# Optimization experiments

Measured on AMD Instinct MI355X. Metric: run time of the kernel, lower is better.

The kernel has to match this reference:

```python
import jax, jax.numpy as jnp
import numpy as np

N_APP = 100000
N_ATTR = 50000
E = 500000
D_IN = 128
D_H = 128
D_OUT = 2


def _sage(h_src, h_dst, src, dst, ew, W_self, W_neigh, b, n_dst):
    # DGL SAGEConv('mean') with edge_weight: m_e = ew_e * h_src[src_e];
    # h_neigh_v = sum_e->v m_e / in_degree(v); out = h_dst@W_self + h_neigh@W_neigh + b
    # (feat_drop=0.2 is identity in eval mode)
    m = h_src[src] * ew[:, None]                                   # [E, d]
    s = jax.ops.segment_sum(m, dst, num_segments=n_dst)            # [n_dst, d]
    deg = jax.ops.segment_sum(jnp.ones_like(ew), dst, num_segments=n_dst)
    h_neigh = s / jnp.maximum(deg, 1.0)[:, None]
    return h_dst @ W_self + h_neigh @ W_neigh + b


def _forward(x_app, x_attr, ew0, ew1, ew2,
             Wself1, Wneigh1, b1, Wself2, Wneigh2, b2, Wc, bc,
             src0, dst0, src1, dst1, src2, dst2):
    # ---- layer 1 (HeteroGraphConv, aggregate='sum' over relations per dst ntype) ----
    h_attr = _sage(x_app, x_attr, src0, dst0, ew0, Wself1[0], Wneigh1[0], b1[0], N_ATTR)
    h_app = (_sage(x_attr, x_app, src1, dst1, ew1, Wself1[1], Wneigh1[1], b1[1], N_APP)
             + _sage(x_app, x_app, src2, dst2, ew2, Wself1[2], Wneigh1[2], b1[2], N_APP))
    h_attr = jax.nn.relu(h_attr)
    h_app = jax.nn.relu(h_app)
    # ---- layer 2 ----
    h_attr2 = _sage(h_app, h_attr, src0, dst0, ew0, Wself2[0], Wneigh2[0], b2[0], N_ATTR)
    h_app2 = (_sage(h_attr, h_app, src1, dst1, ew1, Wself2[1], Wneigh2[1], b2[1], N_APP)
              + _sage(h_app, h_app, src2, dst2, ew2, Wself2[2], Wneigh2[2], b2[2], N_APP))
    del h_attr2  # second layer output on 'attribute' is unused by classify
    # ---- classify on 'application' ----
    return h_app2 @ Wc + bc


def setup_inputs() -> dict:
    key = jax.random.key(0)
    ks = jax.random.split(key, 20)
    sc = 1.0 / np.sqrt(D_H)
    return {
        "x_app": jax.random.normal(ks[0], (N_APP, D_IN), jnp.float32),
        "x_attr": jax.random.normal(ks[1], (N_ATTR, D_IN), jnp.float32),
        "ew0": jax.random.uniform(ks[2], (E,), jnp.float32),
        "ew1": jax.random.uniform(ks[3], (E,), jnp.float32),
        "ew2": jax.random.uniform(ks[4], (E,), jnp.float32),
        "Wself1": jax.random.normal(ks[5], (3, D_IN, D_H), jnp.float32) * sc,
        "Wneigh1": jax.random.normal(ks[6], (3, D_IN, D_H), jnp.float32) * sc,
        "b1": jax.random.normal(ks[7], (3, D_H), jnp.float32) * 0.01,
        "Wself2": jax.random.normal(ks[8], (3, D_H, D_H), jnp.float32) * sc,
        "Wneigh2": jax.random.normal(ks[9], (3, D_H, D_H), jnp.float32) * sc,
        "b2": jax.random.normal(ks[10], (3, D_H), jnp.float32) * 0.01,
        "Wc": jax.random.normal(ks[11], (D_H, D_OUT), jnp.float32) * sc,
        "bc": jax.random.normal(ks[12], (D_OUT,), jnp.float32) * 0.01,
        "src0": jax.random.randint(ks[13], (E,), 0, N_APP, jnp.int32),
        "dst0": jax.random.randint(ks[14], (E,), 0, N_ATTR, jnp.int32),
        "src1": jax.random.randint(ks[15], (E,), 0, N_ATTR, jnp.int32),
        "dst1": jax.random.randint(ks[16], (E,), 0, N_APP, jnp.int32),
        "src2": jax.random.randint(ks[17], (E,), 0, N_APP, jnp.int32),
        "dst2": jax.random.randint(ks[18], (E,), 0, N_APP, jnp.int32),
    }


def reference(x_app, x_attr, ew0, ew1, ew2,
              Wself1, Wneigh1, b1, Wself2, Wneigh2, b2, Wc, bc,
              src0, dst0, src1, dst1, src2, dst2):
    return _forward(x_app, x_attr, ew0, ew1, ew2,
                    Wself1, Wneigh1, b1, Wself2, Wneigh2, b2, Wc, bc,
                    src0, dst0, src1, dst1, src2, dst2)
```

## Files before the change

kernel.cpp:

```cpp
#include <hip/hip_runtime.h>

#define NAPP  100000
#define NATTR 50000
#define NE    500000
#define D     128
#define NTOT  (NATTR + 2 * NAPP)
#define SCHUNK 1024
#define SNB   ((NTOT + SCHUNK - 1) / SCHUNK)
#define EG4   ((NE / 4 + 255) / 256)
#define GB_APP  ((NAPP + 63) / 64)
#define GB_ATTR ((NATTR + 63) / 64)
#define ECAP  1024

typedef __attribute__((ext_vector_type(8))) short bfrag;
typedef __attribute__((ext_vector_type(4))) float f32x4;

__device__ __forceinline__ short bf16_rn(float x) {
    union { float f; unsigned u; } a; a.f = x;
    unsigned r = (a.u + 0x7fffu + ((a.u >> 16) & 1u)) >> 16;
    return (short)r;
}
__device__ __forceinline__ float bf16_to_f(short s) {
    union { float f; unsigned u; } a;
    a.u = ((unsigned)(unsigned short)s) << 16;
    return a.f;
}

__device__ __forceinline__ void split2(float x, float y, unsigned& hw, unsigned& lw) {
    union { float f; unsigned u; } ax, ay;
    ax.f = x; ay.f = y;
    unsigned hx = (ax.u + 0x7fffu + ((ax.u >> 16) & 1u)) >> 16;
    unsigned hy = (ay.u + 0x7fffu + ((ay.u >> 16) & 1u)) >> 16;
    union { unsigned u; float f; } fx, fy;
    fx.u = hx << 16; fy.u = hy << 16;
    union { float f; unsigned u; } rx, ry;
    rx.f = x - fx.f; ry.f = y - fy.f;
    unsigned lx = (rx.u + 0x7fffu + ((rx.u >> 16) & 1u)) >> 16;
    unsigned ly = (ry.u + 0x7fffu + ((ry.u >> 16) & 1u)) >> 16;
    hw = (hy << 16) | (hx & 0xffffu);
    lw = (ly << 16) | (lx & 0xffffu);
}

__global__ __launch_bounds__(256) void hist3_kernel(
        const int* __restrict__ d0, const int* __restrict__ d1, const int* __restrict__ d2,
        int* __restrict__ h0, int* __restrict__ h1, int* __restrict__ h2,
        int* __restrict__ r0, int* __restrict__ r1, int* __restrict__ r2) {
    int b = blockIdx.x;
    int rel = b / EG4;
    int i4 = (b - rel * EG4) * 256 + threadIdx.x;
    if (i4 * 4 >= NE) return;
    const int* dst = (rel == 0) ? d0 : (rel == 1) ? d1 : d2;
    int* h = (rel == 0) ? h0 : (rel == 1) ? h1 : h2;
    int* rk = (rel == 0) ? r0 : (rel == 1) ? r1 : r2;
    int4 d = *((const int4*)dst + i4);
    int4 r;
    r.x = atomicAdd(&h[d.x], 1);
    r.y = atomicAdd(&h[d.y], 1);
    r.z = atomicAdd(&h[d.z], 1);
    r.w = atomicAdd(&h[d.w], 1);
    *((int4*)rk + i4) = r;
}

__global__ __launch_bounds__(256) void scan_partial_kernel(const int* __restrict__ cur,
                                                           int* __restrict__ bsum) {
    int b = blockIdx.x, t = threadIdx.x;
    int4 v = *((const int4*)(cur + b * SCHUNK) + t);
    int s = v.x + v.y + v.z + v.w;
    __shared__ int sd[256];
    sd[t] = s;
    __syncthreads();
    for (int off = 128; off > 0; off >>= 1) {
        if (t < off) sd[t] += sd[t + off];
        __syncthreads();
    }
    if (t == 0) bsum[b] = sd[0];
}

__global__ __launch_bounds__(256) void scan_offsets_kernel(const int* __restrict__ bsum,
        int* __restrict__ boff, int* __restrict__ rp0, int* __restrict__ rp1,
        int* __restrict__ rp2) {
    int t = threadIdx.x;
    int v = (t < SNB) ? bsum[t] : 0;
    __shared__ int sd[256];
    sd[t] = v;
    __syncthreads();
    for (int off = 1; off < 256; off <<= 1) {
        int u = (t >= off) ? sd[t - off] : 0;
        __syncthreads();
        sd[t] += u;
        __syncthreads();
    }
    boff[t] = sd[t] - v;
    if (t == 0) { rp0[NATTR] = NE; rp1[NAPP] = NE; rp2[NAPP] = NE; }
}

__global__ __launch_bounds__(256) void scan_final_kernel(const int* __restrict__ cur,
        const int* __restrict__ boff, int* __restrict__ rp0, int* __restrict__ rp1,
        int* __restrict__ rp2) {
    int b = blockIdx.x, t = threadIdx.x;
    int base = b * SCHUNK + t * 4;
    int4 v = *(const int4*)(cur + base);
    int s = v.x + v.y + v.z + v.w;
    __shared__ int sd[256];
    sd[t] = s;
    __syncthreads();
    for (int off = 1; off < 256; off <<= 1) {
        int u = (t >= off) ? sd[t - off] : 0;
        __syncthreads();
        sd[t] += u;
        __syncthreads();
    }
    int pre = boff[b] + sd[t] - s;
    int ex[4];
    ex[0] = pre;
    ex[1] = ex[0] + v.x;
    ex[2] = ex[1] + v.y;
    ex[3] = ex[2] + v.z;
    #pragma unroll
    for (int i = 0; i < 4; i++) {
        int idx = base + i;
        if (idx < NTOT) {
            int* rp; int loc; int rbase;
            if (idx < NATTR)             { rp = rp0; loc = idx;                 rbase = 0; }
            else if (idx < NATTR + NAPP) { rp = rp1; loc = idx - NATTR;        rbase = NE; }
            else                         { rp = rp2; loc = idx - NATTR - NAPP; rbase = 2 * NE; }
            rp[loc] = ex[i] - rbase;
        }
    }
}

__global__ __launch_bounds__(256) void scatter3_kernel(
        const int* __restrict__ s0, const int* __restrict__ d0, const float* __restrict__ e0,
        const int* __restrict__ r0, const int* __restrict__ rp0, int2* __restrict__ cw0,
        const int* __restrict__ s1, const int* __restrict__ d1, const float* __restrict__ e1,
        const int* __restrict__ r1, const int* __restrict__ rp1, int2* __restrict__ cw1,
        const int* __restrict__ s2, const int* __restrict__ d2, const float* __restrict__ e2,
        const int* __restrict__ r2, const int* __restrict__ rp2, int2* __restrict__ cw2) {
    int b = blockIdx.x;
    int rel = b / EG4;
    int i4 = (b - rel * EG4) * 256 + threadIdx.x;
    if (i4 * 4 >= NE) return;
    const int* src; const int* dst; const float* ew; const int* rk; const int* rp; int2* cw;
    if (rel == 0)      { src = s0; dst = d0; ew = e0; rk = r0; rp = rp0; cw = cw0; }
    else if (rel == 1) { src = s1; dst = d1; ew = e1; rk = r1; rp = rp1; cw = cw1; }
    else               { src = s2; dst = d2; ew = e2; rk = r2; rp = rp2; cw = cw2; }
    int4 s = *((const int4*)src + i4);
    int4 d = *((const int4*)dst + i4);
    float4 e = *((const float4*)ew + i4);
    int4 r = *((const int4*)rk + i4);
    cw[rp[d.x] + r.x] = make_int2(s.x, __float_as_int(e.x));
    cw[rp[d.y] + r.y] = make_int2(s.y, __float_as_int(e.y));
    cw[rp[d.z] + r.z] = make_int2(s.z, __float_as_int(e.z));
    cw[rp[d.w] + r.w] = make_int2(s.w, __float_as_int(e.w));
}

__global__ __launch_bounds__(256) void pack_kernel(
        const float* __restrict__ Wself1, const float* __restrict__ Wneigh1,
        const float* __restrict__ Wself2, const float* __restrict__ Wneigh2,
        const float* __restrict__ b1, const float* __restrict__ b2,
        const float* __restrict__ Wc, const float* __restrict__ bc,
        short* __restrict__ PBh, short* __restrict__ PBl,
        float* __restrict__ b1s, float* __restrict__ b2s,
        float* __restrict__ Cs, float* __restrict__ C1, float* __restrict__ C2,
        float* __restrict__ bconst) {
    int m = blockIdx.x;
    if (m == 8) {
        int tid = threadIdx.x;
        int k = tid >> 1, j = tid & 1;
        const float* Wn1 = Wneigh2 + D * D;
        const float* Wn2 = Wneigh2 + 2 * D * D;
        const float* Ws1 = Wself2 + D * D;
        const float* Ws2 = Wself2 + 2 * D * D;
        float ss = 0.f, s1 = 0.f, s2 = 0.f;
        for (int tt = 0; tt < D; tt++) {
            float wc = Wc[tt * 2 + j];
            ss += (Ws1[k * D + tt] + Ws2[k * D + tt]) * wc;
            s1 += Wn1[k * D + tt] * wc;
            s2 += Wn2[k * D + tt] * wc;
        }
        Cs[tid] = ss; C1[tid] = s1; C2[tid] = s2;
        if (tid < 2) {
            float s = bc[tid];
            for (int tt = 0; tt < D; tt++)
                s += (b2[D + tt] + b2[2 * D + tt]) * Wc[tt * 2 + tid];
            bconst[tid] = s;
        }
        return;
    }
    const float* srcA; const float* srcB = nullptr;
    switch (m) {
        case 0: srcA = Wself1; break;
        case 1: srcA = Wneigh1; break;
        case 2: srcA = Wself1 + D * D; srcB = Wself1 + 2 * D * D; break;
        case 3: srcA = Wneigh1 + D * D; break;
        case 4: srcA = Wneigh1 + 2 * D * D; break;
        case 5: srcA = Wself2 + D * D; srcB = Wself2 + 2 * D * D; break;
        case 6: srcA = Wneigh2 + D * D; break;
        default: srcA = Wneigh2 + 2 * D * D; break;
    }
    short* oh = PBh + (size_t)m * D * D;
    short* ol = PBl + (size_t)m * D * D;
    for (int i = threadIdx.x; i < D * D; i += 256) {
        int k = i >> 7, n = i & 127;
        float v = srcA[i];
        if (srcB) v += srcB[i];
        short hi = bf16_rn(v);
        short lo = bf16_rn(v - bf16_to_f(hi));
        int kc = k >> 5, q = (k >> 3) & 3, j = k & 7, nt = n >> 4, c = n & 15;
        int pos = (((kc * 8 + nt) * 64) + q * 16 + c) * 8 + j;
        oh[pos] = hi;
        ol[pos] = lo;
    }
    if (m == 0 && threadIdx.x < D) {
        int t = threadIdx.x;
        b1s[t] = b1[D + t] + b1[2 * D + t];
        b2s[t] = b2[D + t] + b2[2 * D + t];
    }
}

#define ASTR 128
template<int NG>
__device__ __forceinline__ void fused_body(
        const float* __restrict__ in0, const short* __restrict__ B0h, const short* __restrict__ B0l,
        const float* __restrict__ x1, const int* __restrict__ rp1, const int2* __restrict__ cw1,
        const short* __restrict__ B1h, const short* __restrict__ B1l,
        const float* __restrict__ x2, const int* __restrict__ rp2, const int2* __restrict__ cw2,
        const short* __restrict__ B2h, const short* __restrict__ B2l,
        const float* __restrict__ bias,
        const float* __restrict__ Ccol0, const float* __restrict__ Ccol1,
        float* __restrict__ zo0, float* __restrict__ zo1,
        int nrows, int row0, float* At, int2* eds) {
    const int t = threadIdx.x;
    const int w = t >> 6, lane = t & 63;
    const int q = lane >> 4, c = lane & 15;
    const int myrow = row0 + w * 16 + c;
    const int arow = min(myrow, nrows - 1);

    f32x4 acc[8];
    #pragma unroll
    for (int nt = 0; nt < 8; nt++) acc[nt] = (f32x4){0.f, 0.f, 0.f, 0.f};

    {
        const float* __restrict__ arp = in0 + (size_t)arow * D;
        const bfrag* __restrict__ Bh = (const bfrag*)B0h;
        const bfrag* __restrict__ Bl = (const bfrag*)B0l;
        #pragma unroll
        for (int kc = 0; kc < 4; kc++) {
            float4 a0 = *(const float4*)(arp + kc * 32 + q * 8);
            float4 a1 = *(const float4*)(arp + kc * 32 + q * 8 + 4);
            union { unsigned u[4]; bfrag v; } ahu, alu;
            split2(a0.x, a0.y, ahu.u[0], alu.u[0]);
            split2(a0.z, a0.w, ahu.u[1], alu.u[1]);
            split2(a1.x, a1.y, ahu.u[2], alu.u[2]);
            split2(a1.z, a1.w, ahu.u[3], alu.u[3]);
            bfrag ah = ahu.v, al = alu.v;
            const bfrag* bh = Bh + kc * 512 + lane;
            const bfrag* bl = Bl + kc * 512 + lane;
            #pragma unroll
            for (int nt = 0; nt < 8; nt++) {
                bfrag vh = bh[nt * 64];
                bfrag vl = bl[nt * 64];
                acc[nt] = __builtin_amdgcn_mfma_f32_16x16x32_bf16(ah, vh, acc[nt], 0, 0, 0);
                acc[nt] = __builtin_amdgcn_mfma_f32_16x16x32_bf16(ah, vl, acc[nt], 0, 0, 0);
                acc[nt] = __builtin_amdgcn_mfma_f32_16x16x32_bf16(al, vh, acc[nt], 0, 0, 0);
            }
        }
    }

    const int grp = t >> 5, l32 = t & 31;
    #pragma unroll
    for (int g = 0; g < NG; g++) {
        const float* __restrict__ xs = (g == 0) ? x1 : x2;
        const int* __restrict__ rp   = (g == 0) ? rp1 : rp2;
        const int2* __restrict__ cw  = (g == 0) ? cw1 : cw2;
        const short* __restrict__ Bhp = (g == 0) ? B1h : B2h;
        const short* __restrict__ Blp = (g == 0) ? B1l : B2l;

        if (g > 0) __syncthreads();
        const int eb0 = rp[row0];
        const int eb1 = rp[min(row0 + 64, nrows)];
        const int ecnt = eb1 - eb0;
        const bool staged = (ecnt < ECAP);
        if (staged) {
            for (int i = t; i < ecnt; i += 256) eds[i] = cw[eb0 + i];
            if (t == 0) eds[ecnt] = make_int2(0, 0);
        }
        __syncthreads();

        {
            const int r0g = row0 + grp * 8;
            int bnd[9];
            #pragma unroll
            for (int i = 0; i < 9; i++) bnd[i] = rp[min(r0g + i, nrows)];
            #pragma unroll
            for (int p = 0; p < 4; p++) {
                const int A0 = bnd[2 * p],     A1 = bnd[2 * p + 1];
                const int B0 = bnd[2 * p + 1], B1 = bnd[2 * p + 2];
                float4 aA = make_float4(0.f, 0.f, 0.f, 0.f);
                float4 aB = make_float4(0.f, 0.f, 0.f, 0.f);
                const int lastA = min(max(A1 - 1, A0), NE - 1);
                const int lastB = min(max(B1 - 1, B0), NE - 1);
                int jA = A0, jB = B0;
                while (jA < A1 || jB < B1) {
                    int2 ed[8];
                    if (staged) {
                        #pragma unroll
                        for (int u = 0; u < 4; u++)
                            ed[u] = eds[min(min(jA + u, lastA) - eb0, ecnt)];
                        #pragma unroll
                        for (int u = 0; u < 4; u++)
                            ed[4 + u] = eds[min(min(jB + u, lastB) - eb0, ecnt)];
                    } else {
                        #pragma unroll
                        for (int u = 0; u < 4; u++) ed[u] = cw[min(jA + u, lastA)];
                        #pragma unroll
                        for (int u = 0; u < 4; u++) ed[4 + u] = cw[min(jB + u, lastB)];
                    }
                    float wt[8];
                    #pragma unroll
                    for (int u = 0; u < 4; u++)
                        wt[u] = (jA + u < A1) ? __int_as_float(ed[u].y) : 0.f;
                    #pragma unroll
                    for (int u = 0; u < 4; u++)
                        wt[4 + u] = (jB + u < B1) ? __int_as_float(ed[4 + u].y) : 0.f;
                    float4 v[8];
                    #pragma unroll
                    for (int u = 0; u < 8; u++)
                        v[u] = *(const float4*)(xs + (size_t)ed[u].x * D + l32 * 4);
                    aA.x += wt[0] * v[0].x + wt[1] * v[1].x + wt[2] * v[2].x + wt[3] * v[3].x;
                    aA.y += wt[0] * v[0].y + wt[1] * v[1].y + wt[2] * v[2].y + wt[3] * v[3].y;
                    aA.z += wt[0] * v[0].z + wt[1] * v[1].z + wt[2] * v[2].z + wt[3] * v[3].z;
                    aA.w += wt[0] * v[0].w + wt[1] * v[1].w + wt[2] * v[2].w + wt[3] * v[3].w;
                    aB.x += wt[4] * v[4].x + wt[5] * v[5].x + wt[6] * v[6].x + wt[7] * v[7].x;
                    aB.y += wt[4] * v[4].y + wt[5] * v[5].y + wt[6] * v[6].y + wt[7] * v[7].y;
                    aB.z += wt[4] * v[4].z + wt[5] * v[5].z + wt[6] * v[6].z + wt[7] * v[7].z;
                    aB.w += wt[4] * v[4].w + wt[5] * v[5].w + wt[6] * v[6].w + wt[7] * v[7].w;
                    jA += 4; jB += 4;
                }
                const float invA = 1.0f / (float)max(A1 - A0, 1);
                const float invB = 1.0f / (float)max(B1 - B0, 1);
                aA.x *= invA; aA.y *= invA; aA.z *= invA; aA.w *= invA;
                aB.x *= invB; aB.y *= invB; aB.z *= invB; aB.w *= invB;
                const int lrA = grp * 8 + 2 * p;
                const int lrB = lrA + 1;
                *(float4*)&At[lrA * ASTR + ((l32 ^ ((lrA & 3) << 1)) << 2)] = aA;
                *(float4*)&At[lrB * ASTR + ((l32 ^ ((lrB & 3) << 1)) << 2)] = aB;
            }
        }
        __syncthreads();

        const bfrag* __restrict__ Bh = (const bfrag*)Bhp;
        const bfrag* __restrict__ Bl = (const bfrag*)Blp;
        const int rloc = w * 16 + c;
        const int sw = (rloc & 3) << 1;
        const float* __restrict__ arow_lds = &At[rloc * ASTR];
        #pragma unroll
        for (int kc = 0; kc < 4; kc++) {
            const int g0 = kc * 8 + q * 2;
            float4 a0 = *(const float4*)(arow_lds + ((g0 ^ sw) << 2));
            float4 a1 = *(const float4*)(arow_lds + (((g0 + 1) ^ sw) << 2));
            union { unsigned u[4]; bfrag v; } ahu, alu;
            split2(a0.x, a0.y, ahu.u[0], alu.u[0]);
            split2(a0.z, a0.w, ahu.u[1], alu.u[1]);
            split2(a1.x, a1.y, ahu.u[2], alu.u[2]);
            split2(a1.z, a1.w, ahu.u[3], alu.u[3]);
            bfrag ah = ahu.v, al = alu.v;
            const bfrag* bh = Bh + kc * 512 + lane;
            const bfrag* bl = Bl + kc * 512 + lane;
            #pragma unroll
            for (int nt = 0; nt < 8; nt++) {
                bfrag vh = bh[nt * 64];
                bfrag vl = bl[nt * 64];
                acc[nt] = __builtin_amdgcn_mfma_f32_16x16x32_bf16(ah, vh, acc[nt], 0, 0, 0);
                acc[nt] = __builtin_amdgcn_mfma_f32_16x16x32_bf16(ah, vl, acc[nt], 0, 0, 0);
                acc[nt] = __builtin_amdgcn_mfma_f32_16x16x32_bf16(al, vh, acc[nt], 0, 0, 0);
            }
        }
    }

    float c00[8], c01[8], c10[8], c11[8], bvv[8];
    #pragma unroll
    for (int nt = 0; nt < 8; nt++) {
        float2 v0 = *(const float2*)(Ccol0 + (nt * 16 + c) * 2);
        c00[nt] = v0.x; c01[nt] = v0.y;
        if (NG == 2) {
            float2 v1 = *(const float2*)(Ccol1 + (nt * 16 + c) * 2);
            c10[nt] = v1.x; c11[nt] = v1.y;
        }
        bvv[nt] = bias[nt * 16 + c];
    }
    #pragma unroll
    for (int r = 0; r < 4; r++) {
        int row = row0 + w * 16 + q * 4 + r;
        float s0 = 0.f, s1 = 0.f, t0 = 0.f, t1 = 0.f;
        #pragma unroll
        for (int nt = 0; nt < 8; nt++) {
            float h = fmaxf(acc[nt][r] + bvv[nt], 0.f);
            s0 += h * c00[nt]; s1 += h * c01[nt];
            if (NG == 2) { t0 += h * c10[nt]; t1 += h * c11[nt]; }
        }
        #pragma unroll
        for (int off = 1; off < 16; off <<= 1) {
            s0 += __shfl_xor(s0, off);
            s1 += __shfl_xor(s1, off);
            if (NG == 2) { t0 += __shfl_xor(t0, off); t1 += __shfl_xor(t1, off); }
        }
        if (c == 0 && row < nrows) {
            *(float2*)(zo0 + (size_t)row * 2) = make_float2(s0, s1);
            if (NG == 2) *(float2*)(zo1 + (size_t)row * 2) = make_float2(t0, t1);
        }
    }
}

__global__ __launch_bounds__(256, 4) void fused_all_kernel(
        const float* __restrict__ xapp, const float* __restrict__ xattr,
        const short* __restrict__ PBh, const short* __restrict__ PBl,
        const int* __restrict__ rp0, const int2* __restrict__ cw0,
        const int* __restrict__ rp1, const int2* __restrict__ cw1,
        const int* __restrict__ rp2, const int2* __restrict__ cw2,
        const float* __restrict__ b1, const float* __restrict__ b1s,
        const float* __restrict__ Cs, const float* __restrict__ C2,
        const float* __restrict__ C1,
        float* __restrict__ zs, float* __restrict__ z2, float* __restrict__ za) {
    __shared__ __align__(16) float At[64 * ASTR];
    __shared__ __align__(16) int2 eds[ECAP];
    const size_t MM = (size_t)D * D;
    int b = blockIdx.x;
    if (b < GB_APP) {
        fused_body<2>(xapp, PBh + 2 * MM, PBl + 2 * MM,
                      xattr, rp1, cw1, PBh + 3 * MM, PBl + 3 * MM,
                      xapp,  rp2, cw2, PBh + 4 * MM, PBl + 4 * MM,
                      b1s, Cs, C2, zs, z2, NAPP, b * 64, At, eds);
    } else {
        int bb = b - GB_APP;
        fused_body<1>(xattr, PBh, PBl,
                      xapp, rp0, cw0, PBh + 1 * MM, PBl + 1 * MM,
                      nullptr, nullptr, nullptr, nullptr, nullptr,
                      b1, C1, nullptr, za, nullptr, NATTR, bb * 64, At, eds);
    }
}

__global__ __launch_bounds__(256) void final_out_kernel(
        const float* __restrict__ zs, const float* __restrict__ za,
        const float* __restrict__ z2,
        const int* __restrict__ rp1, const int2* __restrict__ cw1,
        const int* __restrict__ rp2, const int2* __restrict__ cw2,
        const float* __restrict__ bconst, float* __restrict__ out, int n) {
    int r = (blockIdx.x * 256 + threadIdx.x) >> 2;
    int l = threadIdx.x & 3;
    if (r >= n) return;
    int s0 = rp1[r], s1 = rp1[r + 1];
    float q0 = 0.f, q1 = 0.f;
    for (int j = s0 + l; j < s1; j += 4) {
        int2 e = cw1[j];
        float w = __int_as_float(e.y);
        float2 v = *(const float2*)(za + (size_t)e.x * 2);
        q0 += w * v.x; q1 += w * v.y;
    }
    float inv1 = 1.0f / (float)max(s1 - s0, 1);
    float p0 = q0 * inv1, p1 = q1 * inv1;
    s0 = rp2[r]; s1 = rp2[r + 1];
    q0 = 0.f; q1 = 0.f;
    for (int j = s0 + l; j < s1; j += 4) {
        int2 e = cw2[j];
        float w = __int_as_float(e.y);
        float2 v = *(const float2*)(z2 + (size_t)e.x * 2);
        q0 += w * v.x; q1 += w * v.y;
    }
    float inv2 = 1.0f / (float)max(s1 - s0, 1);
    p0 += q0 * inv2; p1 += q1 * inv2;
    #pragma unroll
    for (int off = 1; off < 4; off <<= 1) {
        p0 += __shfl_xor(p0, off);
        p1 += __shfl_xor(p1, off);
    }
    if (l == 0) {
        float2 s = *(const float2*)(zs + (size_t)r * 2);
        out[(size_t)r * 2 + 0] = p0 + s.x + bconst[0];
        out[(size_t)r * 2 + 1] = p1 + s.y + bconst[1];
    }
}

extern "C" void kernel_launch(void* const* d_in, const int* in_sizes, int n_in,
                              void* d_out, int out_size, void* d_ws, size_t ws_size,
                              hipStream_t stream) {
    const float* x_app   = (const float*)d_in[0];
    const float* x_attr  = (const float*)d_in[1];
    const float* ew0     = (const float*)d_in[2];
    const float* ew1     = (const float*)d_in[3];
    const float* ew2     = (const float*)d_in[4];
    const float* Wself1  = (const float*)d_in[5];
    const float* Wneigh1 = (const float*)d_in[6];
    const float* b1      = (const float*)d_in[7];
    const float* Wself2  = (const float*)d_in[8];
    const float* Wneigh2 = (const float*)d_in[9];
    const float* b2      = (const float*)d_in[10];
    const float* Wc      = (const float*)d_in[11];
    const float* bc      = (const float*)d_in[12];
    const int* src0 = (const int*)d_in[13];
    const int* dst0 = (const int*)d_in[14];
    const int* src1 = (const int*)d_in[15];
    const int* dst1 = (const int*)d_in[16];
    const int* src2 = (const int*)d_in[17];
    const int* dst2 = (const int*)d_in[18];
    float* out = (float*)d_out;

    float* ws = (float*)d_ws;
    float* h_attr = ws;
    float* h_app  = h_attr + (size_t)NATTR * D;
    float* b1s    = h_app  + (size_t)NAPP * D;
    float* b2s    = b1s + D;
    float* za     = b2s + D;
    float* zsv    = za + (size_t)NATTR * 2;
    float* z2v    = zsv + (size_t)NAPP * 2;
    float* Cs     = z2v + (size_t)NAPP * 2;
    float* C1     = Cs + 256;
    float* C2     = C1 + 256;
    float* bconst = C2 + 256;
    int* cur  = (int*)(bconst + 4);
    int* cur0 = cur;
    int* cur1 = cur0 + NATTR;
    int* cur2 = cur1 + NAPP;
    int* rp0  = cur + SNB * SCHUNK;
    int* rp1  = rp0 + NATTR + 4;
    int* rp2  = rp1 + NAPP + 4;
    int* bsum = rp2 + NAPP + 4;
    int* boff = bsum + 256;
    int2* cw0 = (int2*)(boff + 256);
    int2* cw1 = cw0 + NE;
    int2* cw2 = cw1 + NE;
    short* PBh = (short*)(cw2 + NE);
    short* PBl = PBh + (size_t)8 * D * D;
    int* rank0 = (int*)h_attr;
    int* rank1 = rank0 + NE;
    int* rank2 = rank1 + NE;

    hipMemsetAsync(cur, 0, (size_t)SNB * SCHUNK * sizeof(int), stream);

    pack_kernel<<<9, 256, 0, stream>>>(Wself1, Wneigh1, Wself2, Wneigh2,
                                       b1, b2, Wc, bc, PBh, PBl, b1s, b2s,
                                       Cs, C1, C2, bconst);

    hist3_kernel<<<3 * EG4, 256, 0, stream>>>(dst0, dst1, dst2, cur0, cur1, cur2,
                                              rank0, rank1, rank2);
    scan_partial_kernel<<<SNB, 256, 0, stream>>>(cur, bsum);
    scan_offsets_kernel<<<1, 256, 0, stream>>>(bsum, boff, rp0, rp1, rp2);
    scan_final_kernel<<<SNB, 256, 0, stream>>>(cur, boff, rp0, rp1, rp2);
    scatter3_kernel<<<3 * EG4, 256, 0, stream>>>(
        src0, dst0, ew0, rank0, rp0, cw0,
        src1, dst1, ew1, rank1, rp1, cw1,
        src2, dst2, ew2, rank2, rp2, cw2);

    fused_all_kernel<<<GB_APP + GB_ATTR, 256, 0, stream>>>(
        x_app, x_attr, PBh, PBl,
        rp0, cw0, rp1, cw1, rp2, cw2,
        b1, b1s, Cs, C2, C1, zsv, z2v, za);

    final_out_kernel<<<((size_t)NAPP * 4 + 255) / 256, 256, 0, stream>>>(
        zsv, za, z2v, rp1, cw1, rp2, cw2, bconst, out, NAPP);
}
```

Measured before the change: 421.3 us.

## Trim CSR build launches: fold memset and scan offsets, use short ranks

Removes the separate hipMemsetAsync by zeroing the histogram inside extra blocks of pack_kernel. It also folds the single-block scan_offsets kernel into scan_final, with every block redoing the small prefix over block sums. Per-edge ranks are stored as 16-bit shorts and each thread handles 8 edges in hist and scatter, cutting launches and rank traffic. Short ranks assume in-degree per node stays under 32768, which holds for random test graphs but not in general. Zeroing cur inside pack_kernel is safe only because hist3 follows it in stream order.

Result: no change. 413.9 us (-1.8%).

```diff
diff --git a/kernel.cpp b/kernel.cpp
--- a/kernel.cpp
+++ b/kernel.cpp
@@ -7,10 +7,11 @@
 #define NTOT  (NATTR + 2 * NAPP)
 #define SCHUNK 1024
 #define SNB   ((NTOT + SCHUNK - 1) / SCHUNK)
-#define EG4   ((NE / 4 + 255) / 256)
+#define EG8   ((NE / 8 + 255) / 256)
 #define GB_APP  ((NAPP + 63) / 64)
 #define GB_ATTR ((NATTR + 63) / 64)
 #define ECAP  1024
+#define ZERO_B 64
 
 typedef __attribute__((ext_vector_type(8))) short bfrag;
 typedef __attribute__((ext_vector_type(4))) float f32x4;
@@ -44,21 +45,26 @@
 __global__ __launch_bounds__(256) void hist3_kernel(
         const int* __restrict__ d0, const int* __restrict__ d1, const int* __restrict__ d2,
         int* __restrict__ h0, int* __restrict__ h1, int* __restrict__ h2,
-        int* __restrict__ r0, int* __restrict__ r1, int* __restrict__ r2) {
+        short* __restrict__ r0, short* __restrict__ r1, short* __restrict__ r2) {
     int b = blockIdx.x;
-    int rel = b / EG4;
-    int i4 = (b - rel * EG4) * 256 + threadIdx.x;
-    if (i4 * 4 >= NE) return;
+    int rel = b / EG8;
+    int i8 = (b - rel * EG8) * 256 + threadIdx.x;
+    if (i8 >= NE / 8) return;
     const int* dst = (rel == 0) ? d0 : (rel == 1) ? d1 : d2;
     int* h = (rel == 0) ? h0 : (rel == 1) ? h1 : h2;
-    int* rk = (rel == 0) ? r0 : (rel == 1) ? r1 : r2;
-    int4 d = *((const int4*)dst + i4);
-    int4 r;
-    r.x = atomicAdd(&h[d.x], 1);
-    r.y = atomicAdd(&h[d.y], 1);
-    r.z = atomicAdd(&h[d.z], 1);
-    r.w = atomicAdd(&h[d.w], 1);
-    *((int4*)rk + i4) = r;
+    short* rk = (rel == 0) ? r0 : (rel == 1) ? r1 : r2;
+    int4 da = *((const int4*)dst + 2 * i8);
+    int4 db = *((const int4*)dst + 2 * i8 + 1);
+    union { short s[8]; int4 v; } u;
+    u.s[0] = (short)atomicAdd(&h[da.x], 1);
+    u.s[1] = (short)atomicAdd(&h[da.y], 1);
+    u.s[2] = (short)atomicAdd(&h[da.z], 1);
+    u.s[3] = (short)atomicAdd(&h[da.w], 1);
+    u.s[4] = (short)atomicAdd(&h[db.x], 1);
+    u.s[5] = (short)atomicAdd(&h[db.y], 1);
+    u.s[6] = (short)atomicAdd(&h[db.z], 1);
+    u.s[7] = (short)atomicAdd(&h[db.w], 1);
+    *((int4*)rk + i8) = u.v;
 }
 
 __global__ __launch_bounds__(256) void scan_partial_kernel(const int* __restrict__ cur,
@@ -76,28 +82,22 @@
     if (t == 0) bsum[b] = sd[0];
 }
 
-__global__ __launch_bounds__(256) void scan_offsets_kernel(const int* __restrict__ bsum,
-        int* __restrict__ boff, int* __restrict__ rp0, int* __restrict__ rp1,
+__global__ __launch_bounds__(256) void scan_final_kernel(const int* __restrict__ cur,
+        const int* __restrict__ bsum, int* __restrict__ rp0, int* __restrict__ rp1,
         int* __restrict__ rp2) {
-    int t = threadIdx.x;
-    int v = (t < SNB) ? bsum[t] : 0;
-    __shared__ int sd[256];
-    sd[t] = v;
+    int b = blockIdx.x, t = threadIdx.x;
+    __shared__ int sb[256];
+    int vb = (t < SNB) ? bsum[t] : 0;
+    sb[t] = vb;
     __syncthreads();
     for (int off = 1; off < 256; off <<= 1) {
-        int u = (t >= off) ? sd[t - off] : 0;
-        __syncthreads();
-        sd[t] += u;
-        __syncthreads();
-    }
-    boff[t] = sd[t] - v;
-    if (t == 0) { rp0[NATTR] = NE; rp1[NAPP] = NE; rp2[NAPP] = NE; }
-}
-
-__global__ __launch_bounds__(256) void scan_final_kernel(const int* __restrict__ cur,
-        const int* __restrict__ boff, int* __restrict__ rp0, int* __restrict__ rp1,
-        int* __restrict__ rp2) {
-    int b = blockIdx.x, t = threadIdx.x;
+        int u = (t >= off) ? sb[t - off] : 0;
+        __syncthreads();
+        sb[t] += u;
+        __syncthreads();
+    }
+    const int boffb = sb[b] - bsum[b];
+    __syncthreads();
     int base = b * SCHUNK + t * 4;
     int4 v = *(const int4*)(cur + base);
     int s = v.x + v.y + v.z + v.w;
@@ -110,7 +110,7 @@
         sd[t] += u;
         __syncthreads();
     }
-    int pre = boff[b] + sd[t] - s;
+    int pre = boffb + sd[t] - s;
     int ex[4];
     ex[0] = pre;
     ex[1] = ex[0] + v.x;
@@ -127,31 +127,40 @@
             rp[loc] = ex[i] - rbase;
         }
     }
+    if (b == 0 && t == 0) { rp0[NATTR] = NE; rp1[NAPP] = NE; rp2[NAPP] = NE; }
 }
 
 __global__ __launch_bounds__(256) void scatter3_kernel(
         const int* __restrict__ s0, const int* __restrict__ d0, const float* __restrict__ e0,
-        const int* __restrict__ r0, const int* __restrict__ rp0, int2* __restrict__ cw0,
+        const short* __restrict__ r0, const int* __restrict__ rp0, int2* __restrict__ cw0,
         const int* __restrict__ s1, const int* __restrict__ d1, const float* __restrict__ e1,
-        const int* __restrict__ r1, const int* __restrict__ rp1, int2* __restrict__ cw1,
+        const short* __restrict__ r1, const int* __restrict__ rp1, int2* __restrict__ cw1,
         const int* __restrict__ s2, const int* __restrict__ d2, const float* __restrict__ e2,
-        const int* __restrict__ r2, const int* __restrict__ rp2, int2* __restrict__ cw2) {
+        const short* __restrict__ r2, const int* __restrict__ rp2, int2* __restrict__ cw2) {
     int b = blockIdx.x;
-    int rel = b / EG4;
-    int i4 = (b - rel * EG4) * 256 + threadIdx.x;
-    if (i4 * 4 >= NE) return;
-    const int* src; const int* dst; const float* ew; const int* rk; const int* rp; int2* cw;
+    int rel = b / EG8;
+    int i8 = (b - rel * EG8) * 256 + threadIdx.x;
+    if (i8 >= NE / 8) return;
+    const int* src; const int* dst; const float* ew; const short* rk; const int* rp; int2* cw;
     if (rel == 0)      { src = s0; dst = d0; ew = e0; rk = r0; rp = rp0; cw = cw0; }
     else if (rel == 1) { src = s1; dst = d1; ew = e1; rk = r1; rp = rp1; cw = cw1; }
     else               { src = s2; dst = d2; ew = e2; rk = r2; rp = rp2; cw = cw2; }
-    int4 s = *((const int4*)src + i4);
-    int4 d = *((const int4*)dst + i4);
-    float4 e = *((const float4*)ew + i4);
-    int4 r = *((const int4*)rk + i4);
-    cw[rp[d.x] + r.x] = make_int2(s.x, __float_as_int(e.x));
-    cw[rp[d.y] + r.y] = make_int2(s.y, __float_as_int(e.y));
-    cw[rp[d.z] + r.z] = make_int2(s.z, __float_as_int(e.z));
-    cw[rp[d.w] + r.w] = make_int2(s.w, __float_as_int(e.w));
+    int4 sa = *((const int4*)src + 2 * i8);
+    int4 sb = *((const int4*)src + 2 * i8 + 1);
+    int4 da = *((const int4*)dst + 2 * i8);
+    int4 db = *((const int4*)dst + 2 * i8 + 1);
+    float4 ea = *((const float4*)ew + 2 * i8);
+    float4 eb = *((const float4*)ew + 2 * i8 + 1);
+    union { short s[8]; int4 v; } u;
+    u.v = *((const int4*)rk + i8);
+    cw[rp[da.x] + u.s[0]] = make_int2(sa.x, __float_as_int(ea.x));
+    cw[rp[da.y] + u.s[1]] = make_int2(sa.y, __float_as_int(ea.y));
+    cw[rp[da.z] + u.s[2]] = make_int2(sa.z, __float_as_int(ea.z));
+    cw[rp[da.w] + u.s[3]] = make_int2(sa.w, __float_as_int(ea.w));
+    cw[rp[db.x] + u.s[4]] = make_int2(sb.x, __float_as_int(eb.x));
+    cw[rp[db.y] + u.s[5]] = make_int2(sb.y, __float_as_int(eb.y));
+    cw[rp[db.z] + u.s[6]] = make_int2(sb.z, __float_as_int(eb.z));
+    cw[rp[db.w] + u.s[7]] = make_int2(sb.w, __float_as_int(eb.w));
 }
 
 __global__ __launch_bounds__(256) void pack_kernel(
@@ -162,8 +171,15 @@
         short* __restrict__ PBh, short* __restrict__ PBl,
         float* __restrict__ b1s, float* __restrict__ b2s,
         float* __restrict__ Cs, float* __restrict__ C1, float* __restrict__ C2,
-        float* __restrict__ bconst) {
+        float* __restrict__ bconst, int* __restrict__ cur) {
     int m = blockIdx.x;
+    if (m >= 9) {
+        int idx = (m - 9) * 256 + threadIdx.x;
+        const int n4 = (SNB * SCHUNK) / 4;
+        for (int i = idx; i < n4; i += ZERO_B * 256)
+            *((int4*)cur + i) = make_int4(0, 0, 0, 0);
+        return;
+    }
     if (m == 8) {
         int tid = threadIdx.x;
         int k = tid >> 1, j = tid & 1;
@@ -531,22 +547,19 @@
     int2* cw2 = cw1 + NE;
     short* PBh = (short*)(cw2 + NE);
     short* PBl = PBh + (size_t)8 * D * D;
-    int* rank0 = (int*)h_attr;
-    int* rank1 = rank0 + NE;
-    int* rank2 = rank1 + NE;
-
-    hipMemsetAsync(cur, 0, (size_t)SNB * SCHUNK * sizeof(int), stream);
-
-    pack_kernel<<<9, 256, 0, stream>>>(Wself1, Wneigh1, Wself2, Wneigh2,
-                                       b1, b2, Wc, bc, PBh, PBl, b1s, b2s,
-                                       Cs, C1, C2, bconst);
-
-    hist3_kernel<<<3 * EG4, 256, 0, stream>>>(dst0, dst1, dst2, cur0, cur1, cur2,
+    short* rank0 = (short*)h_attr;
+    short* rank1 = rank0 + NE;
+    short* rank2 = rank1 + NE;
+
+    pack_kernel<<<9 + ZERO_B, 256, 0, stream>>>(Wself1, Wneigh1, Wself2, Wneigh2,
+                                                b1, b2, Wc, bc, PBh, PBl, b1s, b2s,
+                                                Cs, C1, C2, bconst, cur);
+
+    hist3_kernel<<<3 * EG8, 256, 0, stream>>>(dst0, dst1, dst2, cur0, cur1, cur2,
                                               rank0, rank1, rank2);
     scan_partial_kernel<<<SNB, 256, 0, stream>>>(cur, bsum);
-    scan_offsets_kernel<<<1, 256, 0, stream>>>(bsum, boff, rp0, rp1, rp2);
-    scan_final_kernel<<<SNB, 256, 0, stream>>>(cur, boff, rp0, rp1, rp2);
-    scatter3_kernel<<<3 * EG4, 256, 0, stream>>>(
+    scan_final_kernel<<<SNB, 256, 0, stream>>>(cur, bsum, rp0, rp1, rp2);
+    scatter3_kernel<<<3 * EG8, 256, 0, stream>>>(
         src0, dst0, ew0, rank0, rp0, cw0,
         src1, dst1, ew1, rank1, rp1, cw1,
         src2, dst2, ew2, rank2, rp2, cw2);
```
